# Performance work log

Hardware: AMD Instinct MI355X
Metric: run time of the kernel (lower is better)

## Reference

```python
import jax, jax.numpy as jnp
import numpy as np

B, NMAX, H, C, HID = 256, 512, 256, 64, 512
NEG = jnp.float32(-1e9)

def setup_inputs() -> dict:
    key = jax.random.key(0)
    ks = jax.random.split(key, 12)
    s_in = 1.0 / np.sqrt(2 * H + C)
    s_h = 1.0 / np.sqrt(HID)
    return {
        "nodes_hv": jax.random.normal(ks[0], (B, NMAX, H), jnp.float32),
        "class_cond": jax.random.normal(ks[1], (B, C), jnp.float32),
        "W1": jax.random.normal(ks[2], (2 * H + C, HID), jnp.float32) * s_in,
        "b1": jnp.zeros((HID,), jnp.float32),
        "W2": jax.random.normal(ks[3], (HID, HID), jnp.float32) * s_h,
        "b2": jnp.zeros((HID,), jnp.float32),
        "W3": jax.random.normal(ks[4], (HID, 1), jnp.float32) * s_h,
        "b3": jnp.zeros((1,), jnp.float32),
        "dirns": jax.random.randint(ks[5], (B,), 0, 2, jnp.int32),
        "node_counts": jax.random.randint(ks[6], (B,), NMAX // 2 + 1, NMAX, jnp.int32),
        "dests": jax.random.randint(ks[7], (B,), 0, NMAX // 2, jnp.int32),
    }

def reference(nodes_hv, class_cond, W1, b1, W2, b2, W3, b3, dirns, node_counts, dests):
    Bb, Nmax, Hh = nodes_hv.shape
    D = Nmax - 1  # padded number of candidate destinations
    # per-graph newest node embedding: hv[b, n_b - 1]
    src_idx = (node_counts - 1).astype(jnp.int32)
    src_embed = jnp.take_along_axis(nodes_hv, src_idx[:, None, None], axis=1)  # [B,1,H]
    src_b = jnp.broadcast_to(src_embed, (Bb, D, Hh))
    cand = nodes_hv[:, :D, :]  # candidate (old-node) embeddings, padded
    # dirn == 1: edge new->old, so (src_side, dest_side) = (cand, new); else (new, cand)
    dirn1 = (dirns == 1)[:, None, None]
    side_a = jnp.where(dirn1, cand, src_b)
    side_b = jnp.where(dirn1, src_b, cand)
    cc = jnp.broadcast_to(class_cond[:, None, :], (Bb, D, class_cond.shape[-1]))
    x = jnp.concatenate([side_a, side_b, cc], axis=2)  # [B, D, 2H+C]
    h = jax.nn.relu(jnp.einsum("bdi,ih->bdh", x, W1) + b1)
    h = jax.nn.relu(jnp.einsum("bdi,ih->bdh", h, W2) + b2)
    scores = (jnp.einsum("bdi,io->bdo", h, W3) + b3)[..., 0]  # [B, D]
    # ragged validity: graph b has n_b - 1 candidates
    valid = jnp.arange(D)[None, :] < (node_counts - 1)[:, None]
    scores = jnp.where(valid, scores, NEG)
    logp = jax.nn.log_softmax(scores, axis=1)
    loss = -jnp.take_along_axis(logp, dests[:, None].astype(jnp.int32), axis=1)[:, 0]  # [B]
    return loss
```

## Files before the change

kernel.cpp:

```cpp
#include <hip/hip_runtime.h>
#include <math.h>

#define BB    256
#define NMAX  512
#define HH    256
#define CC    64
#define HID   512
#define NEGV  -1000000000.0f
#define MT    32
#define SA_LD 264
#define SH_LD 520
#define TILE  512
#define KSTR  (32 * TILE)

typedef __attribute__((ext_vector_type(8))) short short8;
typedef __attribute__((ext_vector_type(4))) float floatx4;

__device__ inline ushort f2bf(float x) {
    unsigned u = __float_as_uint(x);
    u = (u + 0x7FFFu + ((u >> 16) & 1u)) >> 16;
    return (ushort)u;
}

__global__ __launch_bounds__(256) void prep_kernel(
    const float* __restrict__ W1, const float* __restrict__ W2,
    ushort* __restrict__ Wt1s, ushort* __restrict__ Wt2s,
    const float* __restrict__ nodes_hv, const float* __restrict__ class_cond,
    const float* __restrict__ b1,
    const int* __restrict__ dirns, const int* __restrict__ node_counts,
    float* __restrict__ v_ws)
{
    const int blk = blockIdx.x;
    const int t = threadIdx.x;

    __shared__ float s_conv[32][68];
    __shared__ float s_src[HH];
    __shared__ float s_cc[CC];

    if (blk < 256) {
        const float* W = (blk < 128) ? W1 : W2;
        ushort* out    = (blk < 128) ? Wt1s : Wt2s;
        const int bb  = blk & 127;
        const int kb  = bb >> 3, ntg = bb & 7;

        {
            const int kl = t >> 3, nn = (t & 7) * 8;
            const float* src = W + (size_t)(kb * 32 + kl) * HID + ntg * 64 + nn;
            *(float4*)&s_conv[kl][nn]     = *(const float4*)src;
            *(float4*)&s_conv[kl][nn + 4] = *(const float4*)(src + 4);
        }
        __syncthreads();

        const int ntl = t >> 6, ls = t & 63;
        const int qs = ls >> 4, l15s = ls & 15;
        short8 o;
        #pragma unroll
        for (int j = 0; j < 8; ++j)
            o[j] = (short)f2bf(s_conv[qs * 8 + j][ntl * 16 + l15s]);
        const int nt = ntg * 4 + ntl;
        *(short8*)(out + ((size_t)(kb * 32 + nt)) * TILE + ls * 8) = o;
    } else {
        const int b = blk - 256;
        const int nc   = node_counts[b];
        const int dirn = dirns[b];
        const int src_idx = nc - 1;

        s_src[t] = nodes_hv[((size_t)b * NMAX + src_idx) * HH + t];
        if (t < CC) s_cc[t] = class_cond[b * CC + t];
        __syncthreads();

        const int srcoff = (dirn == 1) ? HH : 0;

        const int j = 2 * t;
        float acc0 = b1[j];
        float acc1 = b1[j + 1];

        #pragma unroll 4
        for (int r = 0; r < HH; ++r) {
            const float s = s_src[r];
            const float* wp = W1 + (size_t)(srcoff + r) * HID + j;
            acc0 += s * wp[0];
            acc1 += s * wp[1];
        }
        #pragma unroll 4
        for (int c = 0; c < CC; ++c) {
            const float s = s_cc[c];
            const float* wp = W1 + (size_t)(2 * HH + c) * HID + j;
            acc0 += s * wp[0];
            acc1 += s * wp[1];
        }
        v_ws[b * HID + j]     = acc0;
        v_ws[b * HID + j + 1] = acc1;
    }
}

__global__ __launch_bounds__(256, 4) void mlp2(
    const float* __restrict__ nodes_hv,
    const ushort* __restrict__ Wt1s, const ushort* __restrict__ Wt2s,
    const float* __restrict__ b2, const float* __restrict__ W3,
    const float* __restrict__ b3,
    const int* __restrict__ dirns, const int* __restrict__ node_counts,
    const float* __restrict__ v_ws, float* __restrict__ scores)
{
    const int b  = blockIdx.y;
    const int d0 = blockIdx.x * MT;
    const int t  = threadIdx.x;
    const int lane = t & 63, wv = t >> 6;
    const int l15 = lane & 15, q = lane >> 4;

    __shared__ ushort s_u[MT * SH_LD];
    __shared__ float  s_red[4][MT];

    const int nc = node_counts[b];
    const int kb0 = (dirns[b] == 1) ? 0 : 8;

    {
        const float4* src4 = (const float4*)nodes_hv + ((size_t)b * NMAX + d0) * (HH / 4);
        #pragma unroll
        for (int i = 0; i < (MT * HH / 4) / 256; ++i) {
            int idx = t + i * 256;
            int row = idx >> 6, c4 = idx & 63;
            float4 v = src4[idx];
            ushort4 p;
            p.x = f2bf(v.x); p.y = f2bf(v.y); p.z = f2bf(v.z); p.w = f2bf(v.w);
            *(ushort4*)&s_u[row * SA_LD + c4 * 4] = p;
        }
    }
    __syncthreads();

    floatx4 acc[2][8];
    #pragma unroll
    for (int mb = 0; mb < 2; ++mb)
        #pragma unroll
        for (int tn = 0; tn < 8; ++tn)
            acc[mb][tn] = (floatx4){0.f, 0.f, 0.f, 0.f};

    {
        const ushort* wb1 = Wt1s + ((size_t)kb0 * 32 + wv * 8) * TILE + lane * 8;
        #pragma unroll
        for (int ks = 0; ks < 8; ++ks) {
            const ushort* wp = wb1 + (size_t)ks * KSTR;
            short8 bfr[8];
            #pragma unroll
            for (int tn = 0; tn < 8; ++tn)
                bfr[tn] = *(const short8*)(wp + tn * TILE);
            short8 a0 = *(const short8*)&s_u[l15 * SA_LD + ks * 32 + q * 8];
            short8 a1 = *(const short8*)&s_u[(16 + l15) * SA_LD + ks * 32 + q * 8];
            #pragma unroll
            for (int tn = 0; tn < 8; ++tn) {
                acc[0][tn] = __builtin_amdgcn_mfma_f32_16x16x32_bf16(a0, bfr[tn], acc[0][tn], 0, 0, 0);
                acc[1][tn] = __builtin_amdgcn_mfma_f32_16x16x32_bf16(a1, bfr[tn], acc[1][tn], 0, 0, 0);
            }
        }
    }
    __syncthreads();

    const int n0 = wv * 128;

    #pragma unroll
    for (int tn = 0; tn < 8; ++tn) {
        const int n = n0 + tn * 16 + l15;
        const float v = v_ws[b * HID + n];
        #pragma unroll
        for (int mb = 0; mb < 2; ++mb)
            #pragma unroll
            for (int r = 0; r < 4; ++r) {
                float h = acc[mb][tn][r] + v;
                h = h > 0.f ? h : 0.f;
                s_u[(mb * 16 + q * 4 + r) * SH_LD + n] = f2bf(h);
            }
    }
    __syncthreads();

    #pragma unroll
    for (int mb = 0; mb < 2; ++mb)
        #pragma unroll
        for (int tn = 0; tn < 8; ++tn)
            acc[mb][tn] = (floatx4){0.f, 0.f, 0.f, 0.f};
    {
        const ushort* wb2 = Wt2s + ((size_t)wv * 8) * TILE + lane * 8;
        #pragma unroll
        for (int ks = 0; ks < 16; ++ks) {
            const ushort* wp = wb2 + (size_t)ks * KSTR;
            short8 bfr[8];
            #pragma unroll
            for (int tn = 0; tn < 8; ++tn)
                bfr[tn] = *(const short8*)(wp + tn * TILE);
            short8 a0 = *(const short8*)&s_u[l15 * SH_LD + ks * 32 + q * 8];
            short8 a1 = *(const short8*)&s_u[(16 + l15) * SH_LD + ks * 32 + q * 8];
            #pragma unroll
            for (int tn = 0; tn < 8; ++tn) {
                acc[0][tn] = __builtin_amdgcn_mfma_f32_16x16x32_bf16(a0, bfr[tn], acc[0][tn], 0, 0, 0);
                acc[1][tn] = __builtin_amdgcn_mfma_f32_16x16x32_bf16(a1, bfr[tn], acc[1][tn], 0, 0, 0);
            }
        }
    }

    float p[2][4] = {{0.f, 0.f, 0.f, 0.f}, {0.f, 0.f, 0.f, 0.f}};
    #pragma unroll
    for (int tn = 0; tn < 8; ++tn) {
        const int n  = n0 + tn * 16 + l15;
        const float bb = b2[n];
        const float w3 = W3[n];
        #pragma unroll
        for (int mb = 0; mb < 2; ++mb)
            #pragma unroll
            for (int r = 0; r < 4; ++r) {
                float h = acc[mb][tn][r] + bb;
                h = h > 0.f ? h : 0.f;
                p[mb][r] += h * w3;
            }
    }
    #pragma unroll
    for (int mb = 0; mb < 2; ++mb)
        #pragma unroll
        for (int r = 0; r < 4; ++r) {
            float v = p[mb][r];
            v += __shfl_xor(v, 1, 64);
            v += __shfl_xor(v, 2, 64);
            v += __shfl_xor(v, 4, 64);
            v += __shfl_xor(v, 8, 64);
            if (l15 == 0) s_red[wv][mb * 16 + q * 4 + r] = v;
        }
    __syncthreads();
    if (t < MT) {
        const float s = s_red[0][t] + s_red[1][t] + s_red[2][t] + s_red[3][t] + b3[0];
        const int d = d0 + t;
        scores[b * NMAX + d] = (d < nc - 1) ? s : NEGV;
    }
}

__global__ __launch_bounds__(256) void loss_kernel(
    const float* __restrict__ scores, const int* __restrict__ dests,
    float* __restrict__ out)
{
    const int b = blockIdx.x;
    const int t = threadIdx.x;
    __shared__ float red[4];

    const float s0 = scores[b * NMAX + t];
    const float s1 = scores[b * NMAX + t + 256];

    const int lane = t & 63, wv = t >> 6;

    float mx = fmaxf(s0, s1);
    #pragma unroll
    for (int off = 32; off > 0; off >>= 1) mx = fmaxf(mx, __shfl_down(mx, off, 64));
    if (lane == 0) red[wv] = mx;
    __syncthreads();
    mx = fmaxf(fmaxf(red[0], red[1]), fmaxf(red[2], red[3]));
    __syncthreads();

    float e = __expf(s0 - mx) + __expf(s1 - mx);
    #pragma unroll
    for (int off = 32; off > 0; off >>= 1) e += __shfl_down(e, off, 64);
    if (lane == 0) red[wv] = e;
    __syncthreads();

    if (t == 0) {
        const float sum = red[0] + red[1] + red[2] + red[3];
        const float sd = scores[b * NMAX + dests[b]];
        out[b] = -(sd - mx - logf(sum));
    }
}

extern "C" void kernel_launch(void* const* d_in, const int* in_sizes, int n_in,
                              void* d_out, int out_size, void* d_ws, size_t ws_size,
                              hipStream_t stream) {
    const float* nodes_hv    = (const float*)d_in[0];
    const float* class_cond  = (const float*)d_in[1];
    const float* W1          = (const float*)d_in[2];
    const float* b1          = (const float*)d_in[3];
    const float* W2          = (const float*)d_in[4];
    const float* b2          = (const float*)d_in[5];
    const float* W3          = (const float*)d_in[6];
    const float* b3          = (const float*)d_in[7];
    const int*   dirns       = (const int*)d_in[8];
    const int*   node_counts = (const int*)d_in[9];
    const int*   dests       = (const int*)d_in[10];
    float* out = (float*)d_out;

    ushort* Wt1s   = (ushort*)d_ws;
    ushort* Wt2s   = Wt1s + 16 * KSTR;
    float*  v_ws   = (float*)(Wt2s + 16 * KSTR);
    float*  scores = v_ws + BB * HID;

    prep_kernel<<<512, 256, 0, stream>>>(W1, W2, Wt1s, Wt2s,
                                         nodes_hv, class_cond, b1,
                                         dirns, node_counts, v_ws);
    mlp2<<<dim3(NMAX / MT, BB), 256, 0, stream>>>(
        nodes_hv, Wt1s, Wt2s, b2, W3, b3, dirns, node_counts, v_ws, scores);
    loss_kernel<<<BB, 256, 0, stream>>>(scores, dests, out);
}
```

Baseline: 352.6 us.

## Double row tile to 64, skip padded tiles, and swizzle hidden layout in LDS

```diff
diff --git a/kernel.cpp b/kernel.cpp
--- a/kernel.cpp
+++ b/kernel.cpp
@@ -7,9 +7,8 @@
 #define CC    64
 #define HID   512
 #define NEGV  -1000000000.0f
-#define MT    32
+#define MT    64
 #define SA_LD 264
-#define SH_LD 520
 #define TILE  512
 #define KSTR  (32 * TILE)
 
@@ -94,7 +93,7 @@
     }
 }
 
-__global__ __launch_bounds__(256, 4) void mlp2(
+__global__ __launch_bounds__(256, 2) void mlp2(
     const float* __restrict__ nodes_hv,
     const ushort* __restrict__ Wt1s, const ushort* __restrict__ Wt2s,
     const float* __restrict__ b2, const float* __restrict__ W3,
@@ -108,10 +107,15 @@
     const int lane = t & 63, wv = t >> 6;
     const int l15 = lane & 15, q = lane >> 4;
 
-    __shared__ ushort s_u[MT * SH_LD];
-    __shared__ float  s_red[4][MT];
+    __shared__ ushort s_u[32768];
 
     const int nc = node_counts[b];
+
+    if (d0 >= nc - 1) {
+        if (t < MT) scores[b * NMAX + d0 + t] = NEGV;
+        return;
+    }
+
     const int kb0 = (dirns[b] == 1) ? 0 : 8;
 
     {
@@ -128,9 +132,9 @@
     }
     __syncthreads();
 
-    floatx4 acc[2][8];
-    #pragma unroll
-    for (int mb = 0; mb < 2; ++mb)
+    floatx4 acc[4][8];
+    #pragma unroll
+    for (int mb = 0; mb < 4; ++mb)
         #pragma unroll
         for (int tn = 0; tn < 8; ++tn)
             acc[mb][tn] = (floatx4){0.f, 0.f, 0.f, 0.f};
@@ -144,36 +148,44 @@
             #pragma unroll
             for (int tn = 0; tn < 8; ++tn)
                 bfr[tn] = *(const short8*)(wp + tn * TILE);
-            short8 a0 = *(const short8*)&s_u[l15 * SA_LD + ks * 32 + q * 8];
-            short8 a1 = *(const short8*)&s_u[(16 + l15) * SA_LD + ks * 32 + q * 8];
-            #pragma unroll
-            for (int tn = 0; tn < 8; ++tn) {
-                acc[0][tn] = __builtin_amdgcn_mfma_f32_16x16x32_bf16(a0, bfr[tn], acc[0][tn], 0, 0, 0);
-                acc[1][tn] = __builtin_amdgcn_mfma_f32_16x16x32_bf16(a1, bfr[tn], acc[1][tn], 0, 0, 0);
+            short8 a[4];
+            #pragma unroll
+            for (int mb = 0; mb < 4; ++mb)
+                a[mb] = *(const short8*)&s_u[(mb * 16 + l15) * SA_LD + ks * 32 + q * 8];
+            #pragma unroll
+            for (int tn = 0; tn < 8; ++tn)
+                #pragma unroll
+                for (int mb = 0; mb < 4; ++mb)
+                    acc[mb][tn] = __builtin_amdgcn_mfma_f32_16x16x32_bf16(a[mb], bfr[tn], acc[mb][tn], 0, 0, 0);
+        }
+    }
+    __syncthreads();
+
+    const int n0 = wv * 128;
+
+    {
+        const int j_w = l15 & 7;
+        #pragma unroll
+        for (int tn = 0; tn < 8; ++tn) {
+            const int n = n0 + tn * 16 + l15;
+            const float v = v_ws[b * HID + n];
+            const int ks_w = wv * 4 + (tn >> 1);
+            const int qr   = ((tn & 1) << 1) + (l15 >> 3);
+            #pragma unroll
+            for (int mb = 0; mb < 4; ++mb) {
+                #pragma unroll
+                for (int r = 0; r < 4; ++r) {
+                    float h = acc[mb][tn][r] + v;
+                    h = h > 0.f ? h : 0.f;
+                    s_u[((mb * 16 + ks_w) * 64 + qr * 16 + q * 4 + r) * 8 + j_w] = f2bf(h);
+                }
             }
         }
     }
     __syncthreads();
 
-    const int n0 = wv * 128;
-
-    #pragma unroll
-    for (int tn = 0; tn < 8; ++tn) {
-        const int n = n0 + tn * 16 + l15;
-        const float v = v_ws[b * HID + n];
-        #pragma unroll
-        for (int mb = 0; mb < 2; ++mb)
-            #pragma unroll
-            for (int r = 0; r < 4; ++r) {
-                float h = acc[mb][tn][r] + v;
-                h = h > 0.f ? h : 0.f;
-                s_u[(mb * 16 + q * 4 + r) * SH_LD + n] = f2bf(h);
-            }
-    }
-    __syncthreads();
-
-    #pragma unroll
-    for (int mb = 0; mb < 2; ++mb)
+    #pragma unroll
+    for (int mb = 0; mb < 4; ++mb)
         #pragma unroll
         for (int tn = 0; tn < 8; ++tn)
             acc[mb][tn] = (floatx4){0.f, 0.f, 0.f, 0.f};
@@ -186,24 +198,26 @@
             #pragma unroll
             for (int tn = 0; tn < 8; ++tn)
                 bfr[tn] = *(const short8*)(wp + tn * TILE);
-            short8 a0 = *(const short8*)&s_u[l15 * SH_LD + ks * 32 + q * 8];
-            short8 a1 = *(const short8*)&s_u[(16 + l15) * SH_LD + ks * 32 + q * 8];
-            #pragma unroll
-            for (int tn = 0; tn < 8; ++tn) {
-                acc[0][tn] = __builtin_amdgcn_mfma_f32_16x16x32_bf16(a0, bfr[tn], acc[0][tn], 0, 0, 0);
-                acc[1][tn] = __builtin_amdgcn_mfma_f32_16x16x32_bf16(a1, bfr[tn], acc[1][tn], 0, 0, 0);
-            }
-        }
-    }
-
-    float p[2][4] = {{0.f, 0.f, 0.f, 0.f}, {0.f, 0.f, 0.f, 0.f}};
+            short8 a[4];
+            #pragma unroll
+            for (int mb = 0; mb < 4; ++mb)
+                a[mb] = *(const short8*)&s_u[((mb * 16 + ks) * 64 + lane) * 8];
+            #pragma unroll
+            for (int tn = 0; tn < 8; ++tn)
+                #pragma unroll
+                for (int mb = 0; mb < 4; ++mb)
+                    acc[mb][tn] = __builtin_amdgcn_mfma_f32_16x16x32_bf16(a[mb], bfr[tn], acc[mb][tn], 0, 0, 0);
+        }
+    }
+
+    float p[4][4] = {{0,0,0,0},{0,0,0,0},{0,0,0,0},{0,0,0,0}};
     #pragma unroll
     for (int tn = 0; tn < 8; ++tn) {
         const int n  = n0 + tn * 16 + l15;
         const float bb = b2[n];
         const float w3 = W3[n];
         #pragma unroll
-        for (int mb = 0; mb < 2; ++mb)
+        for (int mb = 0; mb < 4; ++mb)
             #pragma unroll
             for (int r = 0; r < 4; ++r) {
                 float h = acc[mb][tn][r] + bb;
@@ -211,8 +225,10 @@
                 p[mb][r] += h * w3;
             }
     }
-    #pragma unroll
-    for (int mb = 0; mb < 2; ++mb)
+    __syncthreads();
+    float* s_red = (float*)s_u;
+    #pragma unroll
+    for (int mb = 0; mb < 4; ++mb)
         #pragma unroll
         for (int r = 0; r < 4; ++r) {
             float v = p[mb][r];
@@ -220,11 +236,12 @@
             v += __shfl_xor(v, 2, 64);
             v += __shfl_xor(v, 4, 64);
             v += __shfl_xor(v, 8, 64);
-            if (l15 == 0) s_red[wv][mb * 16 + q * 4 + r] = v;
+            if (l15 == 0) s_red[wv * MT + mb * 16 + q * 4 + r] = v;
         }
     __syncthreads();
     if (t < MT) {
-        const float s = s_red[0][t] + s_red[1][t] + s_red[2][t] + s_red[3][t] + b3[0];
+        const float s = s_red[0 * MT + t] + s_red[1 * MT + t] +
+                        s_red[2 * MT + t] + s_red[3 * MT + t] + b3[0];
         const int d = d0 + t;
         scores[b * NMAX + d] = (d < nc - 1) ? s : NEGV;
     }
```

Result: no change. 353.1 us (+0.2%).
